# Kernel tuning notes

Measured on AMD Instinct MI355X. Metric: run time of the kernel, lower is better.

## Reference

```python
import jax, jax.numpy as jnp
import numpy as np

NUM_HEADS = 4
HEAD_DIM = 32


def setup_inputs() -> dict:
    key = jax.random.key(0)
    k0, k1, k2 = jax.random.split(key, 3)
    B, S, D = 8, 8192, 128  # d_model == NUM_HEADS * HEAD_DIM (required by source reshape)
    x = jax.random.normal(k0, (B, S, D), dtype=jnp.float32)
    W_qkv = jax.random.normal(k1, (D, 3 * NUM_HEADS * HEAD_DIM), dtype=jnp.float32) * 0.02
    b_qkv = jnp.zeros((3 * NUM_HEADS * HEAD_DIM,), dtype=jnp.float32)
    W_out = jax.random.normal(k2, (S, D), dtype=jnp.float32) * 0.02  # final Dense maps seq axis S -> D
    b_out = jnp.zeros((D,), dtype=jnp.float32)
    return {"x": x, "W_qkv": W_qkv, "b_qkv": b_qkv, "W_out": W_out, "b_out": b_out}


def reference(x, W_qkv, b_qkv, W_out, b_out):
    B, S, D = x.shape
    H, hd = NUM_HEADS, HEAD_DIM
    # fused QKV projection: (B,S,D) -> (B,S,3*H*hd)
    qkv = x @ W_qkv + b_qkv
    qkv = qkv.reshape(B, S, H, 3 * hd)
    q, k, v = jnp.split(qkv, 3, axis=-1)  # each (B,S,H,hd)
    scale = hd ** (-0.5)
    # Faithful to source: q @ k.transpose(0,1,3,2) -> per-position HxH head-mixing scores
    attn = jax.nn.softmax(jnp.einsum("bsqd,bskd->bsqk", q, k) * scale, axis=-1)  # (B,S,H,H)
    out = jnp.einsum("bsqk,bskd->bsqd", attn, v)  # (B,S,H,hd)
    # Faithful to source: reshape(x.shape[0], x.shape[-1], -1) -> (B, D, S) since S*H*hd = S*D
    out = out.reshape(B, D, -1)
    # Final Dense(D) acts on last axis (length S): (B,D,S) @ (S,D) -> (B,D,D)
    return out @ W_out + b_out
```

## Files before the change

kernel.cpp:

```cpp
#include <hip/hip_runtime.h>
#include <math.h>

#define NHEADS 4
#define HDIM   32
#define DMODEL 128
#define SLEN   8192
#define BATCH  8
#define QKVC   384

typedef __bf16 bf16x8 __attribute__((ext_vector_type(8)));
typedef float  f32x4  __attribute__((ext_vector_type(4)));

static __device__ __forceinline__ unsigned short f2bf(float f) {
    union { float f; unsigned int u; } v; v.f = f;
    unsigned int r = (v.u + 0x7FFFu + ((v.u >> 16) & 1u)) >> 16;
    return (unsigned short)r;
}
static __device__ __forceinline__ unsigned int pk2(float a, float b) {
    unsigned short ua = __builtin_bit_cast(unsigned short, (__bf16)a);
    unsigned short ub = __builtin_bit_cast(unsigned short, (__bf16)b);
    return (unsigned int)ua | ((unsigned int)ub << 16);
}
static __device__ __forceinline__ float bf_lo(unsigned int u) {
    union { unsigned int u; float f; } v; v.u = u << 16; return v.f;
}
static __device__ __forceinline__ float bf_hi(unsigned int u) {
    union { unsigned int u; float f; } v; v.u = u & 0xffff0000u; return v.f;
}

__global__ __launch_bounds__(256) void k_conv_wqkv(
    const float* __restrict__ Wqkv, unsigned short* __restrict__ wfb)
{
    const int idx  = blockIdx.x * 256 + threadIdx.x;
    const int lane = idx & 63;
    const int ks   = (idx >> 6) & 3;
    const int rest = idx >> 8;
    const int j    = rest % 6;
    const int w    = rest / 6;
    const int ch   = w * 96 + j * 16 + (lane & 15);
    const int kb   = ks * 32 + (lane >> 4) * 8;
    unsigned short t[8];
    #pragma unroll
    for (int e = 0; e < 8; ++e) t[e] = f2bf(Wqkv[(kb + e) * QKVC + ch]);
    *(uint4*)(wfb + (long)idx * 8) = *(const uint4*)t;
}

__global__ __launch_bounds__(256) void k_conv_wout(
    const float* __restrict__ Wout, unsigned short* __restrict__ Wt)
{
    __shared__ unsigned short ts[128][136];
    const int tid = threadIdx.x;
    const int kb  = blockIdx.x;
    const float* src = Wout + (long)kb * 128 * 128;

    #pragma unroll
    for (int i = 0; i < 64; ++i) {
        const int idx = tid + i * 256;
        const int kk = idx >> 7, n = idx & 127;
        ts[n][kk] = f2bf(src[idx]);
    }
    __syncthreads();
    #pragma unroll
    for (int i = 0; i < 64; ++i) {
        const int idx = tid + i * 256;
        const int n = idx >> 7, kk = idx & 127;
        Wt[(long)n * SLEN + kb * 128 + kk] = ts[n][kk];
    }
}

__global__ __launch_bounds__(256, 3) void k_qkv_attn_mfma(
    const float* __restrict__ x,
    const unsigned short* __restrict__ wfb,
    const float* __restrict__ bqkv,
    unsigned short* __restrict__ attn_out)
{
    __shared__ unsigned short xs[32 * 136];
    __shared__ unsigned short qsm[32 * 384];

    const int tid  = threadIdx.x;
    const int lane = tid & 63;
    const int wave = tid >> 6;
    const int l16  = lane & 15;
    const int lhi  = lane >> 4;
    const long p0  = (long)blockIdx.x * 32;

    {
        const int spos = tid >> 3, sseg = tid & 7;
        const float* src = x + (p0 + spos) * DMODEL + sseg * 16;
        float4 a0 = *(const float4*)(src);
        float4 a1 = *(const float4*)(src + 4);
        float4 a2 = *(const float4*)(src + 8);
        float4 a3 = *(const float4*)(src + 12);
        unsigned int t[8] = {
            pk2(a0.x, a0.y), pk2(a0.z, a0.w), pk2(a1.x, a1.y), pk2(a1.z, a1.w),
            pk2(a2.x, a2.y), pk2(a2.z, a2.w), pk2(a3.x, a3.y), pk2(a3.z, a3.w) };
        *(uint4*)(xs + spos * 136 + sseg * 16)     = ((const uint4*)t)[0];
        *(uint4*)(xs + spos * 136 + sseg * 16 + 8) = ((const uint4*)t)[1];
    }
    __syncthreads();

    {
        f32x4 acc[6][2];
        #pragma unroll
        for (int j = 0; j < 6; ++j)
            #pragma unroll
            for (int nt = 0; nt < 2; ++nt) acc[j][nt] = (f32x4){0.f, 0.f, 0.f, 0.f};

        const unsigned short* wbase = wfb + ((long)(wave * 24) * 64 + lane) * 8;

        #pragma unroll
        for (int ks = 0; ks < 4; ++ks) {
            const bf16x8 xf0 = __builtin_bit_cast(bf16x8,
                *(const uint4*)(xs + l16 * 136 + ks * 32 + lhi * 8));
            const bf16x8 xf1 = __builtin_bit_cast(bf16x8,
                *(const uint4*)(xs + (16 + l16) * 136 + ks * 32 + lhi * 8));
            #pragma unroll
            for (int j = 0; j < 6; ++j) {
                const bf16x8 wj = __builtin_bit_cast(bf16x8,
                    *(const uint4*)(wbase + (j * 4 + ks) * 512));
                acc[j][0] = __builtin_amdgcn_mfma_f32_16x16x32_bf16(wj, xf0, acc[j][0], 0, 0, 0);
                acc[j][1] = __builtin_amdgcn_mfma_f32_16x16x32_bf16(wj, xf1, acc[j][1], 0, 0, 0);
            }
        }

        #pragma unroll
        for (int j = 0; j < 6; ++j) {
            const float4 bb = *(const float4*)(bqkv + wave * 96 + j * 16 + lhi * 4);
            const int c     = wave * 96 + lhi * 4 + j * 16;
            const int chunk = c >> 3;
            const int sub   = c & 7;
            #pragma unroll
            for (int nt = 0; nt < 2; ++nt) {
                const int p = nt * 16 + l16;
                uint2 u;
                u.x = pk2(acc[j][nt][0] + bb.x, acc[j][nt][1] + bb.y);
                u.y = pk2(acc[j][nt][2] + bb.z, acc[j][nt][3] + bb.w);
                *(uint2*)(qsm + p * 384 + (((chunk ^ l16) << 3) + sub)) = u;
            }
        }
    }
    __syncthreads();

    {
        const int p   = tid >> 3;
        const int qh  = (tid >> 1) & 3;
        const int h   = tid & 1;
        const int psw = p & 15;
        const unsigned short* row = qsm + p * 384;
        const float scale = 0.17677669529663687f;

        float qf[16];
        {
            const int qc = qh * 12 + h * 2;
            #pragma unroll
            for (int cc = 0; cc < 2; ++cc) {
                const uint4 qv = *(const uint4*)(row + (((qc + cc) ^ psw) << 3));
                const unsigned int* w = (const unsigned int*)&qv;
                #pragma unroll
                for (int k = 0; k < 4; ++k) {
                    qf[cc * 8 + 2 * k]     = bf_lo(w[k]);
                    qf[cc * 8 + 2 * k + 1] = bf_hi(w[k]);
                }
            }
        }
        float sc[NHEADS];
        #pragma unroll
        for (int kh = 0; kh < NHEADS; ++kh) {
            float s = 0.f;
            const int kc = kh * 12 + 4 + h * 2;
            #pragma unroll
            for (int cc = 0; cc < 2; ++cc) {
                const uint4 kv = *(const uint4*)(row + (((kc + cc) ^ psw) << 3));
                const unsigned int* w = (const unsigned int*)&kv;
                #pragma unroll
                for (int k = 0; k < 4; ++k) {
                    s = fmaf(bf_lo(w[k]), qf[cc * 8 + 2 * k], s);
                    s = fmaf(bf_hi(w[k]), qf[cc * 8 + 2 * k + 1], s);
                }
            }
            sc[kh] = (s + __shfl_xor(s, 1)) * scale;
        }
        const float m = fmaxf(fmaxf(sc[0], sc[1]), fmaxf(sc[2], sc[3]));
        float ew[NHEADS], sum = 0.f;
        #pragma unroll
        for (int kh = 0; kh < NHEADS; ++kh) { ew[kh] = __expf(sc[kh] - m); sum += ew[kh]; }
        const float inv = 1.f / sum;
        #pragma unroll
        for (int kh = 0; kh < NHEADS; ++kh) ew[kh] *= inv;

        float o[16];
        #pragma unroll
        for (int e = 0; e < 16; ++e) o[e] = 0.f;
        #pragma unroll
        for (int kh = 0; kh < NHEADS; ++kh) {
            const float wk = ew[kh];
            const int vc = kh * 12 + 8 + h * 2;
            #pragma unroll
            for (int cc = 0; cc < 2; ++cc) {
                const uint4 vv = *(const uint4*)(row + (((vc + cc) ^ psw) << 3));
                const unsigned int* w = (const unsigned int*)&vv;
                #pragma unroll
                for (int k = 0; k < 4; ++k) {
                    o[cc * 8 + 2 * k]     = fmaf(wk, bf_lo(w[k]), o[cc * 8 + 2 * k]);
                    o[cc * 8 + 2 * k + 1] = fmaf(wk, bf_hi(w[k]), o[cc * 8 + 2 * k + 1]);
                }
            }
        }
        unsigned int ow[8];
        #pragma unroll
        for (int e = 0; e < 8; ++e) ow[e] = pk2(o[2 * e], o[2 * e + 1]);
        unsigned short* dst = attn_out + (p0 + p) * DMODEL + qh * 32 + h * 16;
        *(uint4*)(dst)     = ((const uint4*)ow)[0];
        *(uint4*)(dst + 8) = ((const uint4*)ow)[1];
    }
}

__global__ __launch_bounds__(256, 2) void k_fgemm_mfma(
    const unsigned short* __restrict__ attnBf,
    const unsigned short* __restrict__ WtBf,
    float* __restrict__ P)
{
    __shared__ unsigned short As[64][136];
    __shared__ unsigned short Ws[128][136];

    const int tid   = threadIdx.x;
    const int mtile = blockIdx.x >> 4;
    const int kc    = blockIdx.x & 15;
    const int lane  = tid & 63;
    const int wave  = tid >> 6;
    const int l16   = lane & 15;
    const int lhi   = lane >> 4;

    f32x4 acc[4][2];
    #pragma unroll
    for (int mf = 0; mf < 4; ++mf)
        #pragma unroll
        for (int nt = 0; nt < 2; ++nt) acc[mf][nt] = (f32x4){0.f, 0.f, 0.f, 0.f};

    for (int st = 0; st < 4; ++st) {
        const int k0 = kc * 512 + st * 128;
        __syncthreads();
        #pragma unroll
        for (int i = 0; i < 4; ++i) {
            const int c = tid + i * 256;
            const int m = c >> 4, k8 = c & 15;
            const uint4 v = *(const uint4*)(attnBf + (long)(mtile * 64 + m) * SLEN + k0 + k8 * 8);
            *(uint4*)(&As[m][k8 * 8]) = v;
        }
        #pragma unroll
        for (int i = 0; i < 8; ++i) {
            const int c = tid + i * 256;
            const int n = c >> 4, k8 = c & 15;
            const uint4 v = *(const uint4*)(WtBf + (long)n * SLEN + k0 + k8 * 8);
            *(uint4*)(&Ws[n][k8 * 8]) = v;
        }
        __syncthreads();

        #pragma unroll
        for (int ks = 0; ks < 4; ++ks) {
            const int kk = ks * 32 + lhi * 8;
            bf16x8 af[4], bfr[2];
            #pragma unroll
            for (int mf = 0; mf < 4; ++mf)
                af[mf] = __builtin_bit_cast(bf16x8, *(const uint4*)(&As[mf * 16 + l16][kk]));
            #pragma unroll
            for (int nt = 0; nt < 2; ++nt)
                bfr[nt] = __builtin_bit_cast(bf16x8, *(const uint4*)(&Ws[(wave * 2 + nt) * 16 + l16][kk]));
            #pragma unroll
            for (int mf = 0; mf < 4; ++mf)
                #pragma unroll
                for (int nt = 0; nt < 2; ++nt)
                    acc[mf][nt] = __builtin_amdgcn_mfma_f32_16x16x32_bf16(af[mf], bfr[nt], acc[mf][nt], 0, 0, 0);
        }
    }

    float* Pp = P + ((long)kc * 1024 + mtile * 64) * 128;
    #pragma unroll
    for (int mf = 0; mf < 4; ++mf) {
        #pragma unroll
        for (int nt = 0; nt < 2; ++nt) {
            const int n = (wave * 2 + nt) * 16 + l16;
            #pragma unroll
            for (int r = 0; r < 4; ++r) {
                const int m = mf * 16 + lhi * 4 + r;
                Pp[m * 128 + n] = acc[mf][nt][r];
            }
        }
    }
}

__global__ __launch_bounds__(256) void k_reduce(
    const float* __restrict__ P, const float* __restrict__ bout,
    float* __restrict__ out)
{
    const int idx = blockIdx.x * 256 + threadIdx.x;
    float v = bout[idx & 127];
    #pragma unroll
    for (int kcc = 0; kcc < 16; ++kcc) v += P[(long)kcc * 131072 + idx];
    out[idx] = v;
}

extern "C" void kernel_launch(void* const* d_in, const int* in_sizes, int n_in,
                              void* d_out, int out_size, void* d_ws, size_t ws_size,
                              hipStream_t stream)
{
    const float* x    = (const float*)d_in[0];
    const float* Wqkv = (const float*)d_in[1];
    const float* bqkv = (const float*)d_in[2];
    const float* Wout = (const float*)d_in[3];
    const float* bout = (const float*)d_in[4];
    float* out = (float*)d_out;

    unsigned short* attnBf = (unsigned short*)d_ws;
    unsigned short* WtBf   = (unsigned short*)((char*)d_ws + (16u << 20));
    float*          P      = (float*)((char*)d_ws + (18u << 20));
    unsigned short* wfb    = (unsigned short*)((char*)d_ws + (26u << 20));

    k_conv_wqkv<<<24, 256, 0, stream>>>(Wqkv, wfb);
    k_conv_wout<<<64, 256, 0, stream>>>(Wout, WtBf);
    k_qkv_attn_mfma<<<2048, 256, 0, stream>>>(x, wfb, bqkv, attnBf);
    k_fgemm_mfma<<<256, 256, 0, stream>>>(attnBf, WtBf, P);
    k_reduce<<<(BATCH * DMODEL * DMODEL) / 256, 256, 0, stream>>>(P, bout, out);
}
```

Measured before the change: 46.44 us.

## Merge prep kernels, load x straight into registers, replace split-K reduce with atomics

The two weight-conversion kernels and the output bias initialisation are merged into one prep launch. The separate split-K reduction kernel is removed; the final GEMM now atomically adds its partial tiles into the bias-initialised output. In the QKV kernel, x is loaded from global memory straight into MFMA operand registers instead of being staged through shared memory. That frees LDS and removes a barrier, which allows the occupancy hint to go from 3 to 4. The change saves two launches and the partial-sum buffer traffic, at the cost of fp32 atomic contention and a summation order that is no longer deterministic.

```diff
diff --git a/kernel.cpp b/kernel.cpp
--- a/kernel.cpp
+++ b/kernel.cpp
@@ -28,53 +28,55 @@
     union { unsigned int u; float f; } v; v.u = u & 0xffff0000u; return v.f;
 }
 
-__global__ __launch_bounds__(256) void k_conv_wqkv(
-    const float* __restrict__ Wqkv, unsigned short* __restrict__ wfb)
+__global__ __launch_bounds__(256) void k_prep(
+    const float* __restrict__ Wout, unsigned short* __restrict__ Wt,
+    const float* __restrict__ Wqkv, unsigned short* __restrict__ wfb,
+    const float* __restrict__ bout, float* __restrict__ out)
 {
-    const int idx  = blockIdx.x * 256 + threadIdx.x;
-    const int lane = idx & 63;
-    const int ks   = (idx >> 6) & 3;
-    const int rest = idx >> 8;
-    const int j    = rest % 6;
-    const int w    = rest / 6;
-    const int ch   = w * 96 + j * 16 + (lane & 15);
-    const int kb   = ks * 32 + (lane >> 4) * 8;
-    unsigned short t[8];
-    #pragma unroll
-    for (int e = 0; e < 8; ++e) t[e] = f2bf(Wqkv[(kb + e) * QKVC + ch]);
-    *(uint4*)(wfb + (long)idx * 8) = *(const uint4*)t;
-}
-
-__global__ __launch_bounds__(256) void k_conv_wout(
-    const float* __restrict__ Wout, unsigned short* __restrict__ Wt)
-{
-    __shared__ unsigned short ts[128][136];
     const int tid = threadIdx.x;
-    const int kb  = blockIdx.x;
-    const float* src = Wout + (long)kb * 128 * 128;
-
-    #pragma unroll
-    for (int i = 0; i < 64; ++i) {
-        const int idx = tid + i * 256;
-        const int kk = idx >> 7, n = idx & 127;
-        ts[n][kk] = f2bf(src[idx]);
-    }
-    __syncthreads();
-    #pragma unroll
-    for (int i = 0; i < 64; ++i) {
-        const int idx = tid + i * 256;
-        const int n = idx >> 7, kk = idx & 127;
-        Wt[(long)n * SLEN + kb * 128 + kk] = ts[n][kk];
-    }
-}
-
-__global__ __launch_bounds__(256, 3) void k_qkv_attn_mfma(
+    const int bx  = blockIdx.x;
+
+    if (bx < 64) {
+        __shared__ unsigned short ts[128][136];
+        const float* src = Wout + (long)bx * 128 * 128;
+        #pragma unroll
+        for (int i = 0; i < 64; ++i) {
+            const int idx = tid + i * 256;
+            const int kk = idx >> 7, n = idx & 127;
+            ts[n][kk] = f2bf(src[idx]);
+        }
+        __syncthreads();
+        #pragma unroll
+        for (int i = 0; i < 64; ++i) {
+            const int idx = tid + i * 256;
+            const int n = idx >> 7, kk = idx & 127;
+            Wt[(long)n * SLEN + bx * 128 + kk] = ts[n][kk];
+        }
+    } else if (bx < 88) {
+        const int idx  = (bx - 64) * 256 + tid;
+        const int lane = idx & 63;
+        const int ks   = (idx >> 6) & 3;
+        const int rest = idx >> 8;
+        const int j    = rest % 6;
+        const int w    = rest / 6;
+        const int ch   = w * 96 + j * 16 + (lane & 15);
+        const int kb   = ks * 32 + (lane >> 4) * 8;
+        unsigned short t[8];
+        #pragma unroll
+        for (int e = 0; e < 8; ++e) t[e] = f2bf(Wqkv[(kb + e) * QKVC + ch]);
+        *(uint4*)(wfb + (long)idx * 8) = *(const uint4*)t;
+    } else {
+        const int idx = (bx - 88) * 256 + tid;
+        out[idx] = bout[idx & 127];
+    }
+}
+
+__global__ __launch_bounds__(256, 4) void k_qkv_attn_mfma(
     const float* __restrict__ x,
     const unsigned short* __restrict__ wfb,
     const float* __restrict__ bqkv,
     unsigned short* __restrict__ attn_out)
 {
-    __shared__ unsigned short xs[32 * 136];
     __shared__ unsigned short qsm[32 * 384];
 
     const int tid  = threadIdx.x;
@@ -84,20 +86,22 @@
     const int lhi  = lane >> 4;
     const long p0  = (long)blockIdx.x * 32;
 
+    bf16x8 xb[2][4];
     {
-        const int spos = tid >> 3, sseg = tid & 7;
-        const float* src = x + (p0 + spos) * DMODEL + sseg * 16;
-        float4 a0 = *(const float4*)(src);
-        float4 a1 = *(const float4*)(src + 4);
-        float4 a2 = *(const float4*)(src + 8);
-        float4 a3 = *(const float4*)(src + 12);
-        unsigned int t[8] = {
-            pk2(a0.x, a0.y), pk2(a0.z, a0.w), pk2(a1.x, a1.y), pk2(a1.z, a1.w),
-            pk2(a2.x, a2.y), pk2(a2.z, a2.w), pk2(a3.x, a3.y), pk2(a3.z, a3.w) };
-        *(uint4*)(xs + spos * 136 + sseg * 16)     = ((const uint4*)t)[0];
-        *(uint4*)(xs + spos * 136 + sseg * 16 + 8) = ((const uint4*)t)[1];
-    }
-    __syncthreads();
+        const float* r0 = x + (p0 + l16) * DMODEL + lhi * 8;
+        const float* r1 = r0 + 16 * DMODEL;
+        #pragma unroll
+        for (int ks = 0; ks < 4; ++ks) {
+            float4 a = *(const float4*)(r0 + ks * 32);
+            float4 b = *(const float4*)(r0 + ks * 32 + 4);
+            unsigned int t[4] = { pk2(a.x, a.y), pk2(a.z, a.w), pk2(b.x, b.y), pk2(b.z, b.w) };
+            xb[0][ks] = __builtin_bit_cast(bf16x8, *(const uint4*)t);
+            float4 c = *(const float4*)(r1 + ks * 32);
+            float4 d = *(const float4*)(r1 + ks * 32 + 4);
+            unsigned int u[4] = { pk2(c.x, c.y), pk2(c.z, c.w), pk2(d.x, d.y), pk2(d.z, d.w) };
+            xb[1][ks] = __builtin_bit_cast(bf16x8, *(const uint4*)u);
+        }
+    }
 
     {
         f32x4 acc[6][2];
@@ -107,19 +111,14 @@
             for (int nt = 0; nt < 2; ++nt) acc[j][nt] = (f32x4){0.f, 0.f, 0.f, 0.f};
 
         const unsigned short* wbase = wfb + ((long)(wave * 24) * 64 + lane) * 8;
-
         #pragma unroll
         for (int ks = 0; ks < 4; ++ks) {
-            const bf16x8 xf0 = __builtin_bit_cast(bf16x8,
-                *(const uint4*)(xs + l16 * 136 + ks * 32 + lhi * 8));
-            const bf16x8 xf1 = __builtin_bit_cast(bf16x8,
-                *(const uint4*)(xs + (16 + l16) * 136 + ks * 32 + lhi * 8));
             #pragma unroll
             for (int j = 0; j < 6; ++j) {
                 const bf16x8 wj = __builtin_bit_cast(bf16x8,
                     *(const uint4*)(wbase + (j * 4 + ks) * 512));
-                acc[j][0] = __builtin_amdgcn_mfma_f32_16x16x32_bf16(wj, xf0, acc[j][0], 0, 0, 0);
-                acc[j][1] = __builtin_amdgcn_mfma_f32_16x16x32_bf16(wj, xf1, acc[j][1], 0, 0, 0);
+                acc[j][0] = __builtin_amdgcn_mfma_f32_16x16x32_bf16(wj, xb[0][ks], acc[j][0], 0, 0, 0);
+                acc[j][1] = __builtin_amdgcn_mfma_f32_16x16x32_bf16(wj, xb[1][ks], acc[j][1], 0, 0, 0);
             }
         }
 
@@ -218,7 +217,7 @@
 __global__ __launch_bounds__(256, 2) void k_fgemm_mfma(
     const unsigned short* __restrict__ attnBf,
     const unsigned short* __restrict__ WtBf,
-    float* __restrict__ P)
+    float* __restrict__ out)
 {
     __shared__ unsigned short As[64][136];
     __shared__ unsigned short Ws[128][136];
@@ -274,7 +273,7 @@
         }
     }
 
-    float* Pp = P + ((long)kc * 1024 + mtile * 64) * 128;
+    float* Cp = out + (long)(mtile * 64) * 128;
     #pragma unroll
     for (int mf = 0; mf < 4; ++mf) {
         #pragma unroll
@@ -283,21 +282,10 @@
             #pragma unroll
             for (int r = 0; r < 4; ++r) {
                 const int m = mf * 16 + lhi * 4 + r;
-                Pp[m * 128 + n] = acc[mf][nt][r];
-            }
-        }
-    }
-}
-
-__global__ __launch_bounds__(256) void k_reduce(
-    const float* __restrict__ P, const float* __restrict__ bout,
-    float* __restrict__ out)
-{
-    const int idx = blockIdx.x * 256 + threadIdx.x;
-    float v = bout[idx & 127];
-    #pragma unroll
-    for (int kcc = 0; kcc < 16; ++kcc) v += P[(long)kcc * 131072 + idx];
-    out[idx] = v;
+                atomicAdd(&Cp[m * 128 + n], acc[mf][nt][r]);
+            }
+        }
+    }
 }
 
 extern "C" void kernel_launch(void* const* d_in, const int* in_sizes, int n_in,
@@ -313,12 +301,9 @@
 
     unsigned short* attnBf = (unsigned short*)d_ws;
     unsigned short* WtBf   = (unsigned short*)((char*)d_ws + (16u << 20));
-    float*          P      = (float*)((char*)d_ws + (18u << 20));
-    unsigned short* wfb    = (unsigned short*)((char*)d_ws + (26u << 20));
-
-    k_conv_wqkv<<<24, 256, 0, stream>>>(Wqkv, wfb);
-    k_conv_wout<<<64, 256, 0, stream>>>(Wout, WtBf);
+    unsigned short* wfb    = (unsigned short*)((char*)d_ws + (18u << 20));
+
+    k_prep<<<600, 256, 0, stream>>>(Wout, WtBf, Wqkv, wfb, bout, out);
     k_qkv_attn_mfma<<<2048, 256, 0, stream>>>(x, wfb, bqkv, attnBf);
-    k_fgemm_mfma<<<256, 256, 0, stream>>>(attnBf, WtBf, P);
-    k_reduce<<<(BATCH * DMODEL * DMODEL) / 256, 256, 0, stream>>>(P, bout, out);
-}
+    k_fgemm_mfma<<<256, 256, 0, stream>>>(attnBf, WtBf, out);
+}
```

After: 53.19 us. +14.5%, slower.

## Split fused QKV-attention kernel and merge weight-conversion kernels

Applied to the files above, without the earlier changes.

Merges the two weight-conversion kernels into one launch that branches on block index. It also splits the fused QKV projection plus head-mixing attention kernel into two kernels that pass the QKV tensor through a bf16 global buffer. Dropping the shared-memory QKV stage lowers LDS use per block, which may raise occupancy for the GEMM. The cost is an extra kernel launch and a write and read of a 48 MB intermediate (8x8192x384 bf16).

```diff
diff --git a/kernel.cpp b/kernel.cpp
--- a/kernel.cpp
+++ b/kernel.cpp
@@ -28,54 +28,52 @@
     union { unsigned int u; float f; } v; v.u = u & 0xffff0000u; return v.f;
 }
 
-__global__ __launch_bounds__(256) void k_conv_wqkv(
+__global__ __launch_bounds__(256) void k_prep(
+    const float* __restrict__ Wout, unsigned short* __restrict__ Wt,
     const float* __restrict__ Wqkv, unsigned short* __restrict__ wfb)
 {
-    const int idx  = blockIdx.x * 256 + threadIdx.x;
-    const int lane = idx & 63;
-    const int ks   = (idx >> 6) & 3;
-    const int rest = idx >> 8;
-    const int j    = rest % 6;
-    const int w    = rest / 6;
-    const int ch   = w * 96 + j * 16 + (lane & 15);
-    const int kb   = ks * 32 + (lane >> 4) * 8;
-    unsigned short t[8];
-    #pragma unroll
-    for (int e = 0; e < 8; ++e) t[e] = f2bf(Wqkv[(kb + e) * QKVC + ch]);
-    *(uint4*)(wfb + (long)idx * 8) = *(const uint4*)t;
-}
-
-__global__ __launch_bounds__(256) void k_conv_wout(
-    const float* __restrict__ Wout, unsigned short* __restrict__ Wt)
-{
-    __shared__ unsigned short ts[128][136];
     const int tid = threadIdx.x;
-    const int kb  = blockIdx.x;
-    const float* src = Wout + (long)kb * 128 * 128;
-
-    #pragma unroll
-    for (int i = 0; i < 64; ++i) {
-        const int idx = tid + i * 256;
-        const int kk = idx >> 7, n = idx & 127;
-        ts[n][kk] = f2bf(src[idx]);
-    }
-    __syncthreads();
-    #pragma unroll
-    for (int i = 0; i < 64; ++i) {
-        const int idx = tid + i * 256;
-        const int n = idx >> 7, kk = idx & 127;
-        Wt[(long)n * SLEN + kb * 128 + kk] = ts[n][kk];
-    }
-}
-
-__global__ __launch_bounds__(256, 3) void k_qkv_attn_mfma(
+    const int bx  = blockIdx.x;
+
+    if (bx < 64) {
+        __shared__ unsigned short ts[128][136];
+        const float* src = Wout + (long)bx * 128 * 128;
+        #pragma unroll
+        for (int i = 0; i < 64; ++i) {
+            const int idx = tid + i * 256;
+            const int kk = idx >> 7, n = idx & 127;
+            ts[n][kk] = f2bf(src[idx]);
+        }
+        __syncthreads();
+        #pragma unroll
+        for (int i = 0; i < 64; ++i) {
+            const int idx = tid + i * 256;
+            const int n = idx >> 7, kk = idx & 127;
+            Wt[(long)n * SLEN + bx * 128 + kk] = ts[n][kk];
+        }
+    } else {
+        const int idx  = (bx - 64) * 256 + tid;
+        const int lane = idx & 63;
+        const int ks   = (idx >> 6) & 3;
+        const int rest = idx >> 8;
+        const int j    = rest % 6;
+        const int w    = rest / 6;
+        const int ch   = w * 96 + j * 16 + (lane & 15);
+        const int kb   = ks * 32 + (lane >> 4) * 8;
+        unsigned short t[8];
+        #pragma unroll
+        for (int e = 0; e < 8; ++e) t[e] = f2bf(Wqkv[(kb + e) * QKVC + ch]);
+        *(uint4*)(wfb + (long)idx * 8) = *(const uint4*)t;
+    }
+}
+
+__global__ __launch_bounds__(256, 3) void k_qkv(
     const float* __restrict__ x,
     const unsigned short* __restrict__ wfb,
     const float* __restrict__ bqkv,
-    unsigned short* __restrict__ attn_out)
+    unsigned short* __restrict__ qkvT)
 {
     __shared__ unsigned short xs[32 * 136];
-    __shared__ unsigned short qsm[32 * 384];
 
     const int tid  = threadIdx.x;
     const int lane = tid & 63;
@@ -99,120 +97,119 @@
     }
     __syncthreads();
 
+    f32x4 acc[6][2];
+    #pragma unroll
+    for (int j = 0; j < 6; ++j)
+        #pragma unroll
+        for (int nt = 0; nt < 2; ++nt) acc[j][nt] = (f32x4){0.f, 0.f, 0.f, 0.f};
+
+    const unsigned short* wbase = wfb + ((long)(wave * 24) * 64 + lane) * 8;
+    #pragma unroll
+    for (int ks = 0; ks < 4; ++ks) {
+        const bf16x8 xf0 = __builtin_bit_cast(bf16x8,
+            *(const uint4*)(xs + l16 * 136 + ks * 32 + lhi * 8));
+        const bf16x8 xf1 = __builtin_bit_cast(bf16x8,
+            *(const uint4*)(xs + (16 + l16) * 136 + ks * 32 + lhi * 8));
+        #pragma unroll
+        for (int j = 0; j < 6; ++j) {
+            const bf16x8 wj = __builtin_bit_cast(bf16x8,
+                *(const uint4*)(wbase + (j * 4 + ks) * 512));
+            acc[j][0] = __builtin_amdgcn_mfma_f32_16x16x32_bf16(wj, xf0, acc[j][0], 0, 0, 0);
+            acc[j][1] = __builtin_amdgcn_mfma_f32_16x16x32_bf16(wj, xf1, acc[j][1], 0, 0, 0);
+        }
+    }
+
+    unsigned short* tbase = qkvT + (long)blockIdx.x * 32 * QKVC;
+    #pragma unroll
+    for (int j = 0; j < 6; ++j) {
+        const float4 bb = *(const float4*)(bqkv + wave * 96 + j * 16 + lhi * 4);
+        const int ch = wave * 96 + j * 16 + lhi * 4;
+        #pragma unroll
+        for (int nt = 0; nt < 2; ++nt) {
+            const int p = nt * 16 + l16;
+            uint2 u;
+            u.x = pk2(acc[j][nt][0] + bb.x, acc[j][nt][1] + bb.y);
+            u.y = pk2(acc[j][nt][2] + bb.z, acc[j][nt][3] + bb.w);
+            *(uint2*)(tbase + p * QKVC + ch) = u;
+        }
+    }
+}
+
+__global__ __launch_bounds__(256) void k_attn(
+    const unsigned short* __restrict__ qkvT,
+    unsigned short* __restrict__ attn_out)
+{
+    const int tid = threadIdx.x;
+    const int p   = tid >> 3;
+    const int qh  = (tid >> 1) & 3;
+    const int h   = tid & 1;
+    const unsigned short* row = qkvT + ((long)blockIdx.x * 32 + p) * QKVC;
+    const float scale = 0.17677669529663687f;
+
+    float qf[16];
     {
-        f32x4 acc[6][2];
-        #pragma unroll
-        for (int j = 0; j < 6; ++j)
-            #pragma unroll
-            for (int nt = 0; nt < 2; ++nt) acc[j][nt] = (f32x4){0.f, 0.f, 0.f, 0.f};
-
-        const unsigned short* wbase = wfb + ((long)(wave * 24) * 64 + lane) * 8;
-
-        #pragma unroll
-        for (int ks = 0; ks < 4; ++ks) {
-            const bf16x8 xf0 = __builtin_bit_cast(bf16x8,
-                *(const uint4*)(xs + l16 * 136 + ks * 32 + lhi * 8));
-            const bf16x8 xf1 = __builtin_bit_cast(bf16x8,
-                *(const uint4*)(xs + (16 + l16) * 136 + ks * 32 + lhi * 8));
-            #pragma unroll
-            for (int j = 0; j < 6; ++j) {
-                const bf16x8 wj = __builtin_bit_cast(bf16x8,
-                    *(const uint4*)(wbase + (j * 4 + ks) * 512));
-                acc[j][0] = __builtin_amdgcn_mfma_f32_16x16x32_bf16(wj, xf0, acc[j][0], 0, 0, 0);
-                acc[j][1] = __builtin_amdgcn_mfma_f32_16x16x32_bf16(wj, xf1, acc[j][1], 0, 0, 0);
-            }
-        }
-
-        #pragma unroll
-        for (int j = 0; j < 6; ++j) {
-            const float4 bb = *(const float4*)(bqkv + wave * 96 + j * 16 + lhi * 4);
-            const int c     = wave * 96 + lhi * 4 + j * 16;
-            const int chunk = c >> 3;
-            const int sub   = c & 7;
-            #pragma unroll
-            for (int nt = 0; nt < 2; ++nt) {
-                const int p = nt * 16 + l16;
-                uint2 u;
-                u.x = pk2(acc[j][nt][0] + bb.x, acc[j][nt][1] + bb.y);
-                u.y = pk2(acc[j][nt][2] + bb.z, acc[j][nt][3] + bb.w);
-                *(uint2*)(qsm + p * 384 + (((chunk ^ l16) << 3) + sub)) = u;
-            }
-        }
-    }
-    __syncthreads();
-
-    {
-        const int p   = tid >> 3;
-        const int qh  = (tid >> 1) & 3;
-        const int h   = tid & 1;
-        const int psw = p & 15;
-        const unsigned short* row = qsm + p * 384;
-        const float scale = 0.17677669529663687f;
-
-        float qf[16];
-        {
-            const int qc = qh * 12 + h * 2;
-            #pragma unroll
-            for (int cc = 0; cc < 2; ++cc) {
-                const uint4 qv = *(const uint4*)(row + (((qc + cc) ^ psw) << 3));
-                const unsigned int* w = (const unsigned int*)&qv;
-                #pragma unroll
-                for (int k = 0; k < 4; ++k) {
-                    qf[cc * 8 + 2 * k]     = bf_lo(w[k]);
-                    qf[cc * 8 + 2 * k + 1] = bf_hi(w[k]);
-                }
-            }
-        }
-        float sc[NHEADS];
-        #pragma unroll
-        for (int kh = 0; kh < NHEADS; ++kh) {
-            float s = 0.f;
-            const int kc = kh * 12 + 4 + h * 2;
-            #pragma unroll
-            for (int cc = 0; cc < 2; ++cc) {
-                const uint4 kv = *(const uint4*)(row + (((kc + cc) ^ psw) << 3));
-                const unsigned int* w = (const unsigned int*)&kv;
-                #pragma unroll
-                for (int k = 0; k < 4; ++k) {
-                    s = fmaf(bf_lo(w[k]), qf[cc * 8 + 2 * k], s);
-                    s = fmaf(bf_hi(w[k]), qf[cc * 8 + 2 * k + 1], s);
-                }
-            }
-            sc[kh] = (s + __shfl_xor(s, 1)) * scale;
-        }
-        const float m = fmaxf(fmaxf(sc[0], sc[1]), fmaxf(sc[2], sc[3]));
-        float ew[NHEADS], sum = 0.f;
-        #pragma unroll
-        for (int kh = 0; kh < NHEADS; ++kh) { ew[kh] = __expf(sc[kh] - m); sum += ew[kh]; }
-        const float inv = 1.f / sum;
-        #pragma unroll
-        for (int kh = 0; kh < NHEADS; ++kh) ew[kh] *= inv;
-
-        float o[16];
-        #pragma unroll
-        for (int e = 0; e < 16; ++e) o[e] = 0.f;
-        #pragma unroll
-        for (int kh = 0; kh < NHEADS; ++kh) {
-            const float wk = ew[kh];
-            const int vc = kh * 12 + 8 + h * 2;
-            #pragma unroll
-            for (int cc = 0; cc < 2; ++cc) {
-                const uint4 vv = *(const uint4*)(row + (((vc + cc) ^ psw) << 3));
-                const unsigned int* w = (const unsigned int*)&vv;
-                #pragma unroll
-                for (int k = 0; k < 4; ++k) {
-                    o[cc * 8 + 2 * k]     = fmaf(wk, bf_lo(w[k]), o[cc * 8 + 2 * k]);
-                    o[cc * 8 + 2 * k + 1] = fmaf(wk, bf_hi(w[k]), o[cc * 8 + 2 * k + 1]);
-                }
-            }
-        }
-        unsigned int ow[8];
-        #pragma unroll
-        for (int e = 0; e < 8; ++e) ow[e] = pk2(o[2 * e], o[2 * e + 1]);
-        unsigned short* dst = attn_out + (p0 + p) * DMODEL + qh * 32 + h * 16;
-        *(uint4*)(dst)     = ((const uint4*)ow)[0];
-        *(uint4*)(dst + 8) = ((const uint4*)ow)[1];
-    }
+        const unsigned short* qp = row + qh * 96 + h * 16;
+        const uint4 q0 = *(const uint4*)(qp);
+        const uint4 q1 = *(const uint4*)(qp + 8);
+        const unsigned int* w0 = (const unsigned int*)&q0;
+        const unsigned int* w1 = (const unsigned int*)&q1;
+        #pragma unroll
+        for (int k = 0; k < 4; ++k) {
+            qf[2 * k]     = bf_lo(w0[k]);  qf[2 * k + 1] = bf_hi(w0[k]);
+            qf[8 + 2 * k] = bf_lo(w1[k]);  qf[9 + 2 * k] = bf_hi(w1[k]);
+        }
+    }
+    float sc[NHEADS];
+    #pragma unroll
+    for (int kh = 0; kh < NHEADS; ++kh) {
+        const unsigned short* kp = row + kh * 96 + 32 + h * 16;
+        const uint4 k0 = *(const uint4*)(kp);
+        const uint4 k1 = *(const uint4*)(kp + 8);
+        const unsigned int* w0 = (const unsigned int*)&k0;
+        const unsigned int* w1 = (const unsigned int*)&k1;
+        float s = 0.f;
+        #pragma unroll
+        for (int k = 0; k < 4; ++k) {
+            s = fmaf(bf_lo(w0[k]), qf[2 * k], s);
+            s = fmaf(bf_hi(w0[k]), qf[2 * k + 1], s);
+            s = fmaf(bf_lo(w1[k]), qf[8 + 2 * k], s);
+            s = fmaf(bf_hi(w1[k]), qf[9 + 2 * k], s);
+        }
+        sc[kh] = (s + __shfl_xor(s, 1)) * scale;
+    }
+    const float m = fmaxf(fmaxf(sc[0], sc[1]), fmaxf(sc[2], sc[3]));
+    float ew[NHEADS], sum = 0.f;
+    #pragma unroll
+    for (int kh = 0; kh < NHEADS; ++kh) { ew[kh] = __expf(sc[kh] - m); sum += ew[kh]; }
+    const float inv = 1.f / sum;
+    #pragma unroll
+    for (int kh = 0; kh < NHEADS; ++kh) ew[kh] *= inv;
+
+    float o[16];
+    #pragma unroll
+    for (int e = 0; e < 16; ++e) o[e] = 0.f;
+    #pragma unroll
+    for (int kh = 0; kh < NHEADS; ++kh) {
+        const float wk = ew[kh];
+        const unsigned short* vp = row + kh * 96 + 64 + h * 16;
+        const uint4 v0 = *(const uint4*)(vp);
+        const uint4 v1 = *(const uint4*)(vp + 8);
+        const unsigned int* w0 = (const unsigned int*)&v0;
+        const unsigned int* w1 = (const unsigned int*)&v1;
+        #pragma unroll
+        for (int k = 0; k < 4; ++k) {
+            o[2 * k]     = fmaf(wk, bf_lo(w0[k]), o[2 * k]);
+            o[2 * k + 1] = fmaf(wk, bf_hi(w0[k]), o[2 * k + 1]);
+            o[8 + 2 * k] = fmaf(wk, bf_lo(w1[k]), o[8 + 2 * k]);
+            o[9 + 2 * k] = fmaf(wk, bf_hi(w1[k]), o[9 + 2 * k]);
+        }
+    }
+    unsigned int ow[8];
+    #pragma unroll
+    for (int e = 0; e < 8; ++e) ow[e] = pk2(o[2 * e], o[2 * e + 1]);
+    unsigned short* dst = attn_out + ((long)blockIdx.x * 32 + p) * DMODEL + qh * 32 + h * 16;
+    *(uint4*)(dst)     = ((const uint4*)ow)[0];
+    *(uint4*)(dst + 8) = ((const uint4*)ow)[1];
 }
 
 __global__ __launch_bounds__(256, 2) void k_fgemm_mfma(
@@ -315,10 +312,11 @@
     unsigned short* WtBf   = (unsigned short*)((char*)d_ws + (16u << 20));
     float*          P      = (float*)((char*)d_ws + (18u << 20));
     unsigned short* wfb    = (unsigned short*)((char*)d_ws + (26u << 20));
-
-    k_conv_wqkv<<<24, 256, 0, stream>>>(Wqkv, wfb);
-    k_conv_wout<<<64, 256, 0, stream>>>(Wout, WtBf);
-    k_qkv_attn_mfma<<<2048, 256, 0, stream>>>(x, wfb, bqkv, attnBf);
+    unsigned short* qkvT   = (unsigned short*)((char*)d_ws + (27u << 20));
+
+    k_prep<<<88, 256, 0, stream>>>(Wout, WtBf, Wqkv, wfb);
+    k_qkv<<<2048, 256, 0, stream>>>(x, wfb, bqkv, qkvT);
+    k_attn<<<2048, 256, 0, stream>>>(qkvT, attnBf);
     k_fgemm_mfma<<<256, 256, 0, stream>>>(attnBf, WtBf, P);
-    k_reduce<<<(BATCH * DMODEL * DMODEL) / 256, 256, 0, stream>>>(P, bout, out);
-}
+    k_reduce<<<512, 256, 0, stream>>>(P, bout, out);
+}
```

New measurement: 60.14 us. 1.29x slower.

## Merge weight-prep kernels and process two tiles per block with prefetch

Applied to the files above, without the earlier changes.

The two weight-conversion kernels become one launch, with blocks split by index between the W_out transpose and the W_qkv repack. The fused QKV/attention kernel now handles 64 positions per block as two 32-position tiles. It prefetches the second tile's x into registers while the first tile's MFMA and epilogue run, which halves the grid and overlaps global loads with compute. The cost is more register pressure and extra barriers, and the smaller grid may reduce occupancy or balance.

```diff
diff --git a/kernel.cpp b/kernel.cpp
--- a/kernel.cpp
+++ b/kernel.cpp
@@ -28,43 +28,40 @@
     union { unsigned int u; float f; } v; v.u = u & 0xffff0000u; return v.f;
 }
 
-__global__ __launch_bounds__(256) void k_conv_wqkv(
+__global__ __launch_bounds__(256) void k_prep(
+    const float* __restrict__ Wout, unsigned short* __restrict__ Wt,
     const float* __restrict__ Wqkv, unsigned short* __restrict__ wfb)
 {
-    const int idx  = blockIdx.x * 256 + threadIdx.x;
-    const int lane = idx & 63;
-    const int ks   = (idx >> 6) & 3;
-    const int rest = idx >> 8;
-    const int j    = rest % 6;
-    const int w    = rest / 6;
-    const int ch   = w * 96 + j * 16 + (lane & 15);
-    const int kb   = ks * 32 + (lane >> 4) * 8;
-    unsigned short t[8];
-    #pragma unroll
-    for (int e = 0; e < 8; ++e) t[e] = f2bf(Wqkv[(kb + e) * QKVC + ch]);
-    *(uint4*)(wfb + (long)idx * 8) = *(const uint4*)t;
-}
-
-__global__ __launch_bounds__(256) void k_conv_wout(
-    const float* __restrict__ Wout, unsigned short* __restrict__ Wt)
-{
-    __shared__ unsigned short ts[128][136];
     const int tid = threadIdx.x;
-    const int kb  = blockIdx.x;
-    const float* src = Wout + (long)kb * 128 * 128;
-
-    #pragma unroll
-    for (int i = 0; i < 64; ++i) {
-        const int idx = tid + i * 256;
-        const int kk = idx >> 7, n = idx & 127;
-        ts[n][kk] = f2bf(src[idx]);
-    }
-    __syncthreads();
-    #pragma unroll
-    for (int i = 0; i < 64; ++i) {
-        const int idx = tid + i * 256;
-        const int n = idx >> 7, kk = idx & 127;
-        Wt[(long)n * SLEN + kb * 128 + kk] = ts[n][kk];
+    const int bx  = blockIdx.x;
+
+    if (bx < 64) {
+        __shared__ unsigned short ts[128][136];
+        const float* src = Wout + (long)bx * 128 * 128;
+        #pragma unroll
+        for (int i = 0; i < 64; ++i) {
+            const int idx = tid + i * 256;
+            const int kk = idx >> 7, n = idx & 127;
+            ts[n][kk] = f2bf(src[idx]);
+        }
+        __syncthreads();
+        #pragma unroll
+        for (int i = 0; i < 64; ++i) {
+            const int idx = tid + i * 256;
+            const int n = idx >> 7, kk = idx & 127;
+            Wt[(long)n * SLEN + bx * 128 + kk] = ts[n][kk];
+        }
+    } else {
+        const int idx  = (bx - 64) * 256 + tid;
+        const int lane = idx & 63;
+        const int ks   = (idx >> 6) & 3;
+        const int J    = idx >> 8;
+        const int ch   = J * 16 + (lane & 15);
+        const int kb   = ks * 32 + (lane >> 4) * 8;
+        unsigned short t[8];
+        #pragma unroll
+        for (int e = 0; e < 8; ++e) t[e] = f2bf(Wqkv[(kb + e) * QKVC + ch]);
+        *(uint4*)(wfb + (long)idx * 8) = *(const uint4*)t;
     }
 }
 
@@ -82,24 +79,19 @@
     const int wave = tid >> 6;
     const int l16  = lane & 15;
     const int lhi  = lane >> 4;
-    const long p0  = (long)blockIdx.x * 32;
-
-    {
-        const int spos = tid >> 3, sseg = tid & 7;
-        const float* src = x + (p0 + spos) * DMODEL + sseg * 16;
-        float4 a0 = *(const float4*)(src);
-        float4 a1 = *(const float4*)(src + 4);
-        float4 a2 = *(const float4*)(src + 8);
-        float4 a3 = *(const float4*)(src + 12);
+    const long p00 = (long)blockIdx.x * 64;
+    const int spos = tid >> 3;
+    const int sseg = tid & 7;
+
+    auto stage_write = [&](float4 a0, float4 a1, float4 a2, float4 a3) {
         unsigned int t[8] = {
             pk2(a0.x, a0.y), pk2(a0.z, a0.w), pk2(a1.x, a1.y), pk2(a1.z, a1.w),
             pk2(a2.x, a2.y), pk2(a2.z, a2.w), pk2(a3.x, a3.y), pk2(a3.z, a3.w) };
         *(uint4*)(xs + spos * 136 + sseg * 16)     = ((const uint4*)t)[0];
         *(uint4*)(xs + spos * 136 + sseg * 16 + 8) = ((const uint4*)t)[1];
-    }
-    __syncthreads();
-
-    {
+    };
+
+    auto mfma_phase = [&]() {
         f32x4 acc[6][2];
         #pragma unroll
         for (int j = 0; j < 6; ++j)
@@ -107,7 +99,6 @@
             for (int nt = 0; nt < 2; ++nt) acc[j][nt] = (f32x4){0.f, 0.f, 0.f, 0.f};
 
         const unsigned short* wbase = wfb + ((long)(wave * 24) * 64 + lane) * 8;
-
         #pragma unroll
         for (int ks = 0; ks < 4; ++ks) {
             const bf16x8 xf0 = __builtin_bit_cast(bf16x8,
@@ -122,7 +113,6 @@
                 acc[j][1] = __builtin_amdgcn_mfma_f32_16x16x32_bf16(wj, xf1, acc[j][1], 0, 0, 0);
             }
         }
-
         #pragma unroll
         for (int j = 0; j < 6; ++j) {
             const float4 bb = *(const float4*)(bqkv + wave * 96 + j * 16 + lhi * 4);
@@ -138,10 +128,9 @@
                 *(uint2*)(qsm + p * 384 + (((chunk ^ l16) << 3) + sub)) = u;
             }
         }
-    }
-    __syncthreads();
-
-    {
+    };
+
+    auto epilogue = [&](long p0) {
         const int p   = tid >> 3;
         const int qh  = (tid >> 1) & 3;
         const int h   = tid & 1;
@@ -212,7 +201,31 @@
         unsigned short* dst = attn_out + (p0 + p) * DMODEL + qh * 32 + h * 16;
         *(uint4*)(dst)     = ((const uint4*)ow)[0];
         *(uint4*)(dst + 8) = ((const uint4*)ow)[1];
-    }
+    };
+
+    {
+        const float* src = x + (p00 + spos) * DMODEL + sseg * 16;
+        stage_write(*(const float4*)(src),     *(const float4*)(src + 4),
+                    *(const float4*)(src + 8), *(const float4*)(src + 12));
+    }
+    __syncthreads();
+
+    mfma_phase();
+    float4 xv0, xv1, xv2, xv3;
+    {
+        const float* src = x + (p00 + 32 + spos) * DMODEL + sseg * 16;
+        xv0 = *(const float4*)(src);      xv1 = *(const float4*)(src + 4);
+        xv2 = *(const float4*)(src + 8);  xv3 = *(const float4*)(src + 12);
+    }
+    __syncthreads();
+
+    epilogue(p00);
+    stage_write(xv0, xv1, xv2, xv3);
+    __syncthreads();
+
+    mfma_phase();
+    __syncthreads();
+    epilogue(p00 + 32);
 }
 
 __global__ __launch_bounds__(256, 2) void k_fgemm_mfma(
@@ -316,9 +329,8 @@
     float*          P      = (float*)((char*)d_ws + (18u << 20));
     unsigned short* wfb    = (unsigned short*)((char*)d_ws + (26u << 20));
 
-    k_conv_wqkv<<<24, 256, 0, stream>>>(Wqkv, wfb);
-    k_conv_wout<<<64, 256, 0, stream>>>(Wout, WtBf);
-    k_qkv_attn_mfma<<<2048, 256, 0, stream>>>(x, wfb, bqkv, attnBf);
+    k_prep<<<88, 256, 0, stream>>>(Wout, WtBf, Wqkv, wfb);
+    k_qkv_attn_mfma<<<1024, 256, 0, stream>>>(x, wfb, bqkv, attnBf);
     k_fgemm_mfma<<<256, 256, 0, stream>>>(attnBf, WtBf, P);
-    k_reduce<<<(BATCH * DMODEL * DMODEL) / 256, 256, 0, stream>>>(P, bout, out);
-}
+    k_reduce<<<512, 256, 0, stream>>>(P, bout, out);
+}
```

New measurement: 43.76 us. 5.8% less time.
